# Optimization experiments

Measured on AMD Instinct MI355X. Metric: run time of the kernel, lower is better.

The kernel has to match this reference:

```python
import math
import jax, jax.numpy as jnp
import numpy as np

EMBED_SIZE = 1024
NUM_HEADS = 16
HEAD_DIM = EMBED_SIZE // NUM_HEADS
N, L = 8, 1024
MASK_FILL = -1e3  # value used by masked_fill in the original (NOT -inf)
SCALE = 1.0 / math.sqrt(EMBED_SIZE)  # original divides by embed_size**0.5, not head_dim


def setup_inputs() -> dict:
    key = jax.random.key(0)
    ks = jax.random.split(key, 7)
    values = jax.random.normal(ks[0], (N, L, EMBED_SIZE), dtype=jnp.float32)
    keys_t = jax.random.normal(ks[1], (N, L, EMBED_SIZE), dtype=jnp.float32)
    queries = jax.random.normal(ks[2], (N, L, EMBED_SIZE), dtype=jnp.float32)
    attn_mask = jax.random.randint(ks[3], (1, 1, L, L), 0, 2, dtype=jnp.int32)
    scr_key_padding_mask = jax.random.randint(ks[4], (N, 1, 1, L), 0, 2, dtype=jnp.int32)
    # fc_out: nn.Linear(embed_size, embed_size) with bias
    fc_w = jax.random.normal(ks[5], (EMBED_SIZE, EMBED_SIZE), dtype=jnp.float32) * (1.0 / math.sqrt(EMBED_SIZE))
    fc_b = jax.random.normal(ks[6], (EMBED_SIZE,), dtype=jnp.float32) * 0.01
    return {"values": values, "keys": keys_t, "queries": queries,
            "fc_w": fc_w, "fc_b": fc_b,
            "attn_mask": attn_mask, "scr_key_padding_mask": scr_key_padding_mask}


def reference(values, keys, queries, fc_w, fc_b, attn_mask, scr_key_padding_mask):
    n, q_len, e = queries.shape
    k_len = keys.shape[1]
    h, d = NUM_HEADS, HEAD_DIM
    # NOTE: the original defines per-head Linear projections but never applies them
    v = values.reshape(n, k_len, h, d)
    k = keys.reshape(n, k_len, h, d)
    q = queries.reshape(n, q_len, h, d)
    energy = jnp.einsum('nqhd,nkhd->nhqk', q, k)  # [n, h, q, k]
    am = attn_mask[:, :, :k_len, :k_len]
    energy = jnp.where(am == 0, MASK_FILL, energy)
    energy = jnp.where(scr_key_padding_mask == 0, MASK_FILL, energy)
    attention = jax.nn.softmax(energy * SCALE, axis=3)
    out = jnp.einsum('nhql,nlhd->nqhd', attention, v).reshape(n, q_len, h * d)
    return out @ fc_w.T + fc_b
```

## Files before the change

### kernel.cpp

```cpp
#include <hip/hip_runtime.h>

#define L_SEQ 1024
#define EMB 1024
#define NH 16
#define HD 64

typedef _Float16 half8 __attribute__((ext_vector_type(8)));
typedef _Float16 half4v __attribute__((ext_vector_type(4)));
typedef float f32x4 __attribute__((ext_vector_type(4)));
typedef float fvec4 __attribute__((ext_vector_type(4)));
typedef unsigned int u32;
typedef unsigned long long u64;

constexpr float C2 = 0.045084220027780106f;
constexpr float F2 = -45.08422002778011f;

constexpr int PP = 72;

__device__ __forceinline__ void async16(const void* g, void* l) {
    __builtin_amdgcn_global_load_lds((const __attribute__((address_space(1))) u32*)g,
                                     (__attribute__((address_space(3))) u32*)l, 16, 0, 0);
}

__global__ void pack_mask_kernel(const int* __restrict__ am, u32* __restrict__ bits) {
    const int i = blockIdx.x * 256 + threadIdx.x;
    const int lane = threadIdx.x & 63;
    u64 b = __ballot(am[i] != 0);
    if (lane == 0)       bits[i >> 5] = (u32)b;
    else if (lane == 32) bits[i >> 5] = (u32)(b >> 32);
}

__global__ void combine_mask_kernel(const u32* __restrict__ abits,
                                    const u32* __restrict__ pbits,
                                    u32* __restrict__ cmb) {
    const int tid = threadIdx.x;
    const int w = tid & 31, qq = tid >> 5;
    const int q = blockIdx.x * 8 + qq;
    const u32 a = abits[q * 32 + w];
#pragma unroll
    for (int n = 0; n < 8; ++n)
        cmb[((size_t)(n * L_SEQ) + q) * 32 + w] = a & pbits[n * 32 + w];
}

__global__ void convert_w_kernel(const float* __restrict__ w, _Float16* __restrict__ o) {
    size_t i = ((size_t)blockIdx.x * blockDim.x + threadIdx.x) * 4;
    fvec4 v = *(const fvec4*)(w + i);
    half4v h;
#pragma unroll
    for (int j = 0; j < 4; ++j) h[j] = (_Float16)v[j];
    *(half4v*)(o + i) = h;
}

__global__ __launch_bounds__(256) void cvt_kv_kernel(
    const float* __restrict__ keys, const float* __restrict__ values,
    const int* __restrict__ pad_mask,
    _Float16* __restrict__ K16, _Float16* __restrict__ Vt16, u32* __restrict__ pbits)
{
    __shared__ __align__(16) _Float16 Vt[64 * PP];
    const int tid = threadIdx.x;
    const int kt = blockIdx.x, h = blockIdx.y, n = blockIdx.z;
    const int kbase = kt * 64;
    const int r = tid >> 2, c0 = (tid & 3) * 16;
    const int nh = n * NH + h;

    {
        const float* src = keys + ((size_t)(n * L_SEQ + kbase + r)) * EMB + h * HD + c0;
        fvec4 a0 = *(const fvec4*)(src),     a1 = *(const fvec4*)(src + 4);
        fvec4 a2 = *(const fvec4*)(src + 8), a3 = *(const fvec4*)(src + 12);
        half8 o0, o1;
#pragma unroll
        for (int j = 0; j < 4; ++j) {
            o0[j] = (_Float16)a0[j]; o0[j + 4] = (_Float16)a1[j];
            o1[j] = (_Float16)a2[j]; o1[j + 4] = (_Float16)a3[j];
        }
        _Float16* dst = K16 + ((size_t)nh * L_SEQ + kbase + r) * HD + c0;
        *(half8*)dst = o0; *(half8*)(dst + 8) = o1;
    }
    {
        const float* src = values + ((size_t)(n * L_SEQ + kbase + r)) * EMB + h * HD + c0;
        fvec4 vv[4];
        vv[0] = *(const fvec4*)(src);     vv[1] = *(const fvec4*)(src + 4);
        vv[2] = *(const fvec4*)(src + 8); vv[3] = *(const fvec4*)(src + 12);
#pragma unroll
        for (int i = 0; i < 16; ++i)
            Vt[(c0 + i) * PP + r] = (_Float16)vv[i >> 2][i & 3];
    }
    if (blockIdx.y == 0 && tid < 64) {
        u64 b = __ballot(pad_mask[(size_t)n * L_SEQ + kbase + tid] != 0);
        if (tid == 0)       pbits[n * 32 + kt * 2]     = (u32)b;
        else if (tid == 32) pbits[n * 32 + kt * 2 + 1] = (u32)(b >> 32);
    }
    __syncthreads();
    {
        const int d = tid >> 2, k0 = (tid & 3) * 16;
        half8 v0 = *(const half8*)(&Vt[d * PP + k0]);
        half8 v1 = *(const half8*)(&Vt[d * PP + k0 + 8]);
        _Float16* dst = Vt16 + ((size_t)nh * HD + d) * L_SEQ + kbase + k0;
        *(half8*)dst = v0; *(half8*)(dst + 8) = v1;
    }
}

__global__ __launch_bounds__(256, 3) void attn_kernel(
    const _Float16* __restrict__ K16, const _Float16* __restrict__ Vt16,
    const float* __restrict__ queries, const u32* __restrict__ cmb,
    _Float16* __restrict__ out_f16)
{
    __shared__ __align__(16) _Float16 K_lds[2][64 * 64];
    __shared__ __align__(16) _Float16 V_lds[2][64 * 64];
    __shared__ __align__(16) _Float16 P_lds[128 * PP];

    const int tid = threadIdx.x;
    const int lane = tid & 63;
    const int wave = tid >> 6;
    const int l16 = lane & 15;
    const int quad = lane >> 4;
    const int bid = blockIdx.x;
    const int nh = bid & 127, qt = bid >> 7;
    const int n = nh >> 4, h = nh & 15;
    const int qbase = qt * 128;
    const int xr = l16 & 7;

    half8 qf[2][2];
#pragma unroll
    for (int s = 0; s < 2; ++s) {
        const int qrow = qbase + wave * 32 + s * 16 + l16;
        const float* qp = queries + ((size_t)(n * L_SEQ + qrow)) * EMB + h * HD;
#pragma unroll
        for (int t = 0; t < 2; ++t) {
            fvec4 a = *(const fvec4*)(qp + t * 32 + quad * 8);
            fvec4 b = *(const fvec4*)(qp + t * 32 + quad * 8 + 4);
#pragma unroll
            for (int j = 0; j < 4; ++j) {
                qf[s][t][j]     = (_Float16)(a[j] * C2);
                qf[s][t][j + 4] = (_Float16)(b[j] * C2);
            }
        }
    }

    f32x4 Ov[2][4];
#pragma unroll
    for (int s = 0; s < 2; ++s)
#pragma unroll
        for (int dt = 0; dt < 4; ++dt) Ov[s][dt] = (f32x4){0.f, 0.f, 0.f, 0.f};
    float lsum[2] = {0.f, 0.f};

    const _Float16* Kt_base = K16 + (size_t)nh * L_SEQ * HD;
    const _Float16* Vt_base = Vt16 + (size_t)nh * HD * L_SEQ;
    const int gch = (lane & 7) ^ ((lane >> 3) & 7);
    const int drow = (lane >> 3);
    const u32* mrow0 = cmb + ((size_t)(n * L_SEQ) + qbase + wave * 32 + l16) * 32;
    const u32* mrow1 = mrow0 + 16 * 32;

#pragma unroll
    for (int s2 = 0; s2 < 2; ++s2) {
        const int row = wave * 16 + s2 * 8 + drow;
        async16(Kt_base + (size_t)row * HD + gch * 8, &K_lds[0][(wave * 16 + s2 * 8) * 64]);
        async16(Vt_base + (size_t)row * L_SEQ + gch * 8, &V_lds[0][(wave * 16 + s2 * 8) * 64]);
    }

    for (int kt = 0; kt < L_SEQ / 64; ++kt) {
        const int cb = kt & 1;
        __syncthreads();

        if (kt < 15) {
            const int kb2 = (kt + 1) * 64;
#pragma unroll
            for (int s2 = 0; s2 < 2; ++s2) {
                const int row = wave * 16 + s2 * 8 + drow;
                async16(Kt_base + (size_t)(kb2 + row) * HD + gch * 8,
                        &K_lds[cb ^ 1][(wave * 16 + s2 * 8) * 64]);
                async16(Vt_base + (size_t)row * L_SEQ + kb2 + gch * 8,
                        &V_lds[cb ^ 1][(wave * 16 + s2 * 8) * 64]);
            }
        }
        const u32 w0a = mrow0[kt * 2], w1a = mrow0[kt * 2 + 1];
        const u32 w0b = mrow1[kt * 2], w1b = mrow1[kt * 2 + 1];

        f32x4 S[2][4];
#pragma unroll
        for (int s = 0; s < 2; ++s)
#pragma unroll
            for (int tj = 0; tj < 4; ++tj) S[s][tj] = (f32x4){0.f, 0.f, 0.f, 0.f};
#pragma unroll
        for (int tj = 0; tj < 4; ++tj) {
            const _Float16* kr = &K_lds[cb][(tj * 16 + l16) * 64];
            const int c0 = (quad ^ xr) * 8;
            half8 k0 = *(const half8*)(kr + c0);
            half8 k1 = *(const half8*)(kr + (c0 ^ 32));
            S[0][tj] = __builtin_amdgcn_mfma_f32_16x16x32_f16(k0, qf[0][0], S[0][tj], 0, 0, 0);
            S[0][tj] = __builtin_amdgcn_mfma_f32_16x16x32_f16(k1, qf[0][1], S[0][tj], 0, 0, 0);
            S[1][tj] = __builtin_amdgcn_mfma_f32_16x16x32_f16(k0, qf[1][0], S[1][tj], 0, 0, 0);
            S[1][tj] = __builtin_amdgcn_mfma_f32_16x16x32_f16(k1, qf[1][1], S[1][tj], 0, 0, 0);
        }

#pragma unroll
        for (int s = 0; s < 2; ++s) {
            const u32 pw0 = s ? w0b : w0a, pw1 = s ? w1b : w1a;
#pragma unroll
            for (int tj = 0; tj < 4; ++tj) {
                const u32 m4 = ((tj & 2) ? pw1 : pw0) >> ((tj & 1) * 16 + quad * 4);
                float p[4];
#pragma unroll
                for (int reg = 0; reg < 4; ++reg) {
                    const float e = ((m4 >> reg) & 1u) ? S[s][tj][reg] : F2;
                    p[reg] = __builtin_amdgcn_exp2f(e);
                }
                lsum[s] += (p[0] + p[1]) + (p[2] + p[3]);
                half4v hp = {(_Float16)p[0], (_Float16)p[1], (_Float16)p[2], (_Float16)p[3]};
                *(half4v*)(&P_lds[(wave * 32 + s * 16 + l16) * PP + tj * 16 + quad * 4]) = hp;
            }
        }

        half8 pf0[2], pf1[2];
#pragma unroll
        for (int t = 0; t < 2; ++t) {
            pf0[t] = *(const half8*)(&P_lds[(wave * 32 + l16) * PP + t * 32 + quad * 8]);
            pf1[t] = *(const half8*)(&P_lds[(wave * 32 + 16 + l16) * PP + t * 32 + quad * 8]);
        }
#pragma unroll
        for (int t = 0; t < 2; ++t) {
            const int c0 = ((t * 4 + quad) ^ xr) * 8;
#pragma unroll
            for (int dt = 0; dt < 4; ++dt) {
                half8 vf = *(const half8*)(&V_lds[cb][(dt * 16 + l16) * 64 + c0]);
                Ov[0][dt] = __builtin_amdgcn_mfma_f32_16x16x32_f16(pf0[t], vf, Ov[0][dt], 0, 0, 0);
                Ov[1][dt] = __builtin_amdgcn_mfma_f32_16x16x32_f16(pf1[t], vf, Ov[1][dt], 0, 0, 0);
            }
        }
    }

#pragma unroll
    for (int s = 0; s < 2; ++s) {
        lsum[s] += __shfl_xor(lsum[s], 16);
        lsum[s] += __shfl_xor(lsum[s], 32);
    }
#pragma unroll
    for (int s = 0; s < 2; ++s)
#pragma unroll
        for (int reg = 0; reg < 4; ++reg) {
            const float linv = 1.0f / __shfl(lsum[s], quad * 4 + reg);
            const int qrow = qbase + wave * 32 + s * 16 + quad * 4 + reg;
            _Float16* op = out_f16 + ((size_t)(n * L_SEQ + qrow)) * EMB + h * HD;
#pragma unroll
            for (int dt = 0; dt < 4; ++dt)
                op[dt * 16 + l16] = (_Float16)(Ov[s][dt][reg] * linv);
        }
}

__global__ __launch_bounds__(256, 3) void fc_kernel(
    const _Float16* __restrict__ A, const _Float16* __restrict__ W,
    const float* __restrict__ bias, float* __restrict__ C)
{
    __shared__ __align__(16) _Float16 As[128 * 64];
    __shared__ __align__(16) _Float16 Ws[128 * 64];

    const int tid = threadIdx.x;
    const int lane = tid & 63;
    const int wv = tid >> 6;
    const int l16 = lane & 15;
    const int quad = lane >> 4;
    const int wm = (wv >> 1) * 64, wn = (wv & 1) * 64;
    const int Mb = blockIdx.x * 128, Nb = blockIdx.y * 128;
    const int gch = (lane & 7) ^ ((lane >> 3) & 7);
    const int drow = lane >> 3;
    const int xr = l16 & 7;

    f32x4 acc[4][4];
#pragma unroll
    for (int i = 0; i < 4; ++i)
#pragma unroll
        for (int j = 0; j < 4; ++j) acc[i][j] = (f32x4){0.f, 0.f, 0.f, 0.f};

    for (int k0 = 0; k0 < EMB; k0 += 64) {
        __syncthreads();
#pragma unroll
        for (int s = 0; s < 4; ++s) {
            const int row = wv * 32 + s * 8 + drow;
            async16(A + (size_t)(Mb + row) * EMB + k0 + gch * 8, &As[(wv * 32 + s * 8) * 64]);
            async16(W + (size_t)(Nb + row) * EMB + k0 + gch * 8, &Ws[(wv * 32 + s * 8) * 64]);
        }
        __syncthreads();

#pragma unroll
        for (int t = 0; t < 2; ++t) {
            half8 af[4], bf[4];
            const int c0 = ((t * 4 + quad) ^ xr) * 8;
#pragma unroll
            for (int i = 0; i < 4; ++i) {
                af[i] = *(const half8*)(&As[(wm + i * 16 + l16) * 64 + c0]);
                bf[i] = *(const half8*)(&Ws[(wn + i * 16 + l16) * 64 + c0]);
            }
#pragma unroll
            for (int i = 0; i < 4; ++i)
#pragma unroll
                for (int j = 0; j < 4; ++j)
                    acc[i][j] = __builtin_amdgcn_mfma_f32_16x16x32_f16(af[i], bf[j], acc[i][j], 0, 0, 0);
        }
    }

#pragma unroll
    for (int i = 0; i < 4; ++i) {
        const int m = Mb + wm + i * 16 + quad * 4;
#pragma unroll
        for (int j = 0; j < 4; ++j) {
            const int jc = Nb + wn + j * 16 + l16;
            const float b = bias[jc];
#pragma unroll
            for (int reg = 0; reg < 4; ++reg)
                C[(size_t)(m + reg) * EMB + jc] = acc[i][j][reg] + b;
        }
    }
}

extern "C" void kernel_launch(void* const* d_in, const int* in_sizes, int n_in,
                              void* d_out, int out_size, void* d_ws, size_t ws_size,
                              hipStream_t stream) {
    const float* values  = (const float*)d_in[0];
    const float* keys    = (const float*)d_in[1];
    const float* queries = (const float*)d_in[2];
    const float* fc_w    = (const float*)d_in[3];
    const float* fc_b    = (const float*)d_in[4];
    const int*   amask   = (const int*)d_in[5];
    const int*   pmask   = (const int*)d_in[6];
    float* out = (float*)d_out;

    char* w = (char*)d_ws;
    _Float16* attn_out = (_Float16*)w;
    _Float16* w_f16    = (_Float16*)(w + (size_t)16 * 1024 * 1024);
    u32*      abits    = (u32*)(w + (size_t)18 * 1024 * 1024);
    u32*      pbits    = (u32*)(w + (size_t)18 * 1024 * 1024 + 512 * 1024);
    u32*      cmb      = (u32*)(w + (size_t)19 * 1024 * 1024);
    _Float16* K16      = (_Float16*)(w + (size_t)20 * 1024 * 1024);
    _Float16* Vt16     = (_Float16*)(w + (size_t)36 * 1024 * 1024);

    pack_mask_kernel<<<4096, 256, 0, stream>>>(amask, abits);
    convert_w_kernel<<<1024, 256, 0, stream>>>(fc_w, w_f16);
    cvt_kv_kernel<<<dim3(16, 16, 8), 256, 0, stream>>>(keys, values, pmask, K16, Vt16, pbits);
    combine_mask_kernel<<<128, 256, 0, stream>>>(abits, pbits, cmb);
    attn_kernel<<<1024, 256, 0, stream>>>(K16, Vt16, queries, cmb, attn_out);
    fc_kernel<<<dim3(64, 8), 256, 0, stream>>>(attn_out, w_f16, fc_b, out);
}
```

Before: 242.6 us.

## Keep softmax probabilities in registers by computing transposed PV product

Drops the P_lds staging buffer. The attention-times-V product is now computed as O^T = V^T·P^T with 16x16x16 MFMAs, so the exp results held in the score accumulator layout feed straight in as the B operand. Masking now exponentiates unconditionally and zeroes masked lanes with a bitwise AND, instead of selecting a fill constant. The output is written as packed half4 stores, and launch bounds rise to 4 blocks per SIMD because LDS use is lower. The cost is switching from the K=32 to the K=16 MFMA instruction, which may have lower throughput on this chip. Masked entries also become exactly zero, so a fully masked row would now divide by zero rather than give the reference's uniform weights.

```diff
diff --git a/kernel.cpp b/kernel.cpp
--- a/kernel.cpp
+++ b/kernel.cpp
@@ -13,7 +13,6 @@
 typedef unsigned long long u64;
 
 constexpr float C2 = 0.045084220027780106f;
-constexpr float F2 = -45.08422002778011f;
 
 constexpr int PP = 72;
 
@@ -100,14 +99,13 @@
     }
 }
 
-__global__ __launch_bounds__(256, 3) void attn_kernel(
+__global__ __launch_bounds__(256, 4) void attn_kernel(
     const _Float16* __restrict__ K16, const _Float16* __restrict__ Vt16,
     const float* __restrict__ queries, const u32* __restrict__ cmb,
     _Float16* __restrict__ out_f16)
 {
     __shared__ __align__(16) _Float16 K_lds[2][64 * 64];
     __shared__ __align__(16) _Float16 V_lds[2][64 * 64];
-    __shared__ __align__(16) _Float16 P_lds[128 * PP];
 
     const int tid = threadIdx.x;
     const int lane = tid & 63;
@@ -137,11 +135,11 @@
         }
     }
 
-    f32x4 Ov[2][4];
+    f32x4 Ot[2][4];
 #pragma unroll
     for (int s = 0; s < 2; ++s)
 #pragma unroll
-        for (int dt = 0; dt < 4; ++dt) Ov[s][dt] = (f32x4){0.f, 0.f, 0.f, 0.f};
+        for (int dt = 0; dt < 4; ++dt) Ot[s][dt] = (f32x4){0.f, 0.f, 0.f, 0.f};
     float lsum[2] = {0.f, 0.f};
 
     const _Float16* Kt_base = K16 + (size_t)nh * L_SEQ * HD;
@@ -150,6 +148,8 @@
     const int drow = (lane >> 3);
     const u32* mrow0 = cmb + ((size_t)(n * L_SEQ) + qbase + wave * 32 + l16) * 32;
     const u32* mrow1 = mrow0 + 16 * 32;
+
+    const int voff_base = l16 * 64 + (quad & 1) * 4;
 
 #pragma unroll
     for (int s2 = 0; s2 < 2; ++s2) {
@@ -194,37 +194,32 @@
         }
 
 #pragma unroll
-        for (int s = 0; s < 2; ++s) {
-            const u32 pw0 = s ? w0b : w0a, pw1 = s ? w1b : w1a;
-#pragma unroll
-            for (int tj = 0; tj < 4; ++tj) {
+        for (int tj = 0; tj < 4; ++tj) {
+            const int c = tj * 2 + (quad >> 1);
+            half4v vf[4];
+#pragma unroll
+            for (int dt = 0; dt < 4; ++dt)
+                vf[dt] = *(const half4v*)(&V_lds[cb][dt * 16 * 64 + voff_base + ((c ^ xr) * 8)]);
+
+            half4v hp[2];
+#pragma unroll
+            for (int s = 0; s < 2; ++s) {
+                const u32 pw0 = s ? w0b : w0a, pw1 = s ? w1b : w1a;
                 const u32 m4 = ((tj & 2) ? pw1 : pw0) >> ((tj & 1) * 16 + quad * 4);
                 float p[4];
 #pragma unroll
                 for (int reg = 0; reg < 4; ++reg) {
-                    const float e = ((m4 >> reg) & 1u) ? S[s][tj][reg] : F2;
-                    p[reg] = __builtin_amdgcn_exp2f(e);
+                    float z = __builtin_amdgcn_exp2f(S[s][tj][reg]);
+                    int zi = __float_as_int(z) & (-(int)((m4 >> reg) & 1u));
+                    p[reg] = __int_as_float(zi);
                 }
                 lsum[s] += (p[0] + p[1]) + (p[2] + p[3]);
-                half4v hp = {(_Float16)p[0], (_Float16)p[1], (_Float16)p[2], (_Float16)p[3]};
-                *(half4v*)(&P_lds[(wave * 32 + s * 16 + l16) * PP + tj * 16 + quad * 4]) = hp;
-            }
-        }
-
-        half8 pf0[2], pf1[2];
-#pragma unroll
-        for (int t = 0; t < 2; ++t) {
-            pf0[t] = *(const half8*)(&P_lds[(wave * 32 + l16) * PP + t * 32 + quad * 8]);
-            pf1[t] = *(const half8*)(&P_lds[(wave * 32 + 16 + l16) * PP + t * 32 + quad * 8]);
-        }
-#pragma unroll
-        for (int t = 0; t < 2; ++t) {
-            const int c0 = ((t * 4 + quad) ^ xr) * 8;
+                hp[s] = half4v{(_Float16)p[0], (_Float16)p[1], (_Float16)p[2], (_Float16)p[3]};
+            }
 #pragma unroll
             for (int dt = 0; dt < 4; ++dt) {
-                half8 vf = *(const half8*)(&V_lds[cb][(dt * 16 + l16) * 64 + c0]);
-                Ov[0][dt] = __builtin_amdgcn_mfma_f32_16x16x32_f16(pf0[t], vf, Ov[0][dt], 0, 0, 0);
-                Ov[1][dt] = __builtin_amdgcn_mfma_f32_16x16x32_f16(pf1[t], vf, Ov[1][dt], 0, 0, 0);
+                Ot[0][dt] = __builtin_amdgcn_mfma_f32_16x16x16f16(vf[dt], hp[0], Ot[0][dt], 0, 0, 0);
+                Ot[1][dt] = __builtin_amdgcn_mfma_f32_16x16x16f16(vf[dt], hp[1], Ot[1][dt], 0, 0, 0);
             }
         }
     }
@@ -235,16 +230,18 @@
         lsum[s] += __shfl_xor(lsum[s], 32);
     }
 #pragma unroll
-    for (int s = 0; s < 2; ++s)
-#pragma unroll
-        for (int reg = 0; reg < 4; ++reg) {
-            const float linv = 1.0f / __shfl(lsum[s], quad * 4 + reg);
-            const int qrow = qbase + wave * 32 + s * 16 + quad * 4 + reg;
-            _Float16* op = out_f16 + ((size_t)(n * L_SEQ + qrow)) * EMB + h * HD;
-#pragma unroll
-            for (int dt = 0; dt < 4; ++dt)
-                op[dt * 16 + l16] = (_Float16)(Ov[s][dt][reg] * linv);
-        }
+    for (int s = 0; s < 2; ++s) {
+        const float linv = 1.0f / lsum[s];
+        const int q = qbase + wave * 32 + s * 16 + l16;
+        _Float16* op = out_f16 + ((size_t)(n * L_SEQ + q)) * EMB + h * HD;
+#pragma unroll
+        for (int dt = 0; dt < 4; ++dt) {
+            half4v o;
+#pragma unroll
+            for (int reg = 0; reg < 4; ++reg) o[reg] = (_Float16)(Ot[s][dt][reg] * linv);
+            *(half4v*)(op + dt * 16 + quad * 4) = o;
+        }
+    }
 }
 
 __global__ __launch_bounds__(256, 3) void fc_kernel(
```

After: 269.9 us. 11.3% more time.
